# Kernel optimization log

Measured on AMD Instinct MI355X. Metric: run time of the kernel, lower is better.

Reference implementation:

```python
import jax, jax.numpy as jnp
import numpy as np

N, S, Q, P = 100000, 64, 50, 3  # pauli words, heads, qubits, pauli basis
EPS = 1e-12  # F.normalize clamp


def setup_inputs() -> dict:
    key = jax.random.key(0)
    k1, k2, k3, k4 = jax.random.split(key, 4)
    return {
        "batch_pauli_tensor": jax.random.uniform(k1, (N, Q, P), dtype=jnp.float32),
        "batch_coeff": jax.random.normal(k2, (N,), dtype=jnp.float32),
        "heads_param": jax.random.normal(k3, (S, Q, P), dtype=jnp.float32),
        "head_ratios_param": jax.random.normal(k4, (S,), dtype=jnp.float32),
    }


def reference(batch_pauli_tensor, batch_coeff, heads_param, head_ratios_param):
    s = heads_param.shape[0]
    heads = jax.nn.softplus(heads_param * 20.0)
    heads = heads / jnp.maximum(jnp.sum(heads, axis=-1, keepdims=True), EPS)
    hr = jax.nn.softplus(head_ratios_param * 20.0)
    hr = hr / jnp.maximum(jnp.sum(hr), EPS)
    hr = (hr + 0.001 / s) / 1.001
    # coverage: per-(word, head, qubit) match prob -> product over qubits -> ratio-weighted sum
    cov = jnp.einsum('nqp,sqp->nsq', batch_pauli_tensor, heads)  # [n, s, q]
    cov = jnp.prod(cov, axis=-1)                                 # [n, s]
    cov = jnp.einsum('s,ns->n', hr, cov)                         # [n]
    # variance loss
    return jnp.sum(batch_coeff ** 2 / cov)
```

## Files before the change

### kernel.cpp

```cpp
#include <hip/hip_runtime.h>
#include <math.h>

#define N_Q 50
#define N_P 3
#define N_S 64
#define ROW 150
#define BLK_ROWS 128
#define THREADS 256
#define SCHUNK 16

#define WS_CNT_OFF 6272
#define WS_HP_OFF 6336
#define WS_HRV_OFF 44736

__device__ __forceinline__ float softplus20(float x) {
    float z = x * 20.0f;
    return fmaxf(z, 0.0f) + log1pf(expf(-fabsf(z)));
}

__global__ void precompute_kernel(const float* __restrict__ heads_param,
                                  const float* __restrict__ hr_param,
                                  float* __restrict__ HP,
                                  float* __restrict__ hrv,
                                  int* __restrict__ cnt) {
    const int tid = threadIdx.x;
    if (blockIdx.x == 0) {
        if (tid == 0) *cnt = 0;
        if (tid < N_S) {
            float sp = softplus20(hr_param[tid]);
            float tot = sp;
            #pragma unroll
            for (int off = 32; off; off >>= 1) tot += __shfl_xor(tot, off);
            float hr = sp / fmaxf(tot, 1e-12f);
            hrv[tid] = (hr + 0.001f / (float)N_S) / 1.001f;
        }
    }
    int idx = blockIdx.x * blockDim.x + tid;
    if (idx < N_S * N_Q) {
        int q = idx / N_S;
        int s = idx - q * N_S;
        const float* hp = heads_param + ((size_t)s * N_Q + q) * N_P;
        float sp0 = softplus20(hp[0]);
        float sp1 = softplus20(hp[1]);
        float sp2 = softplus20(hp[2]);
        float denom = fmaxf(sp0 + sp1 + sp2, 1e-12f);
        float* o = HP + ((size_t)q * N_S + s) * 3;
        o[0] = sp0 / denom;
        o[1] = sp1 / denom;
        o[2] = sp2 / denom;
    }
}

__device__ __forceinline__ void computeQ2(const float4* __restrict__ Hq,
                                          float a0, float a1, float a2,
                                          float c0, float c1, float c2,
                                          float (&p)[SCHUNK], float (&p2)[SCHUNK]) {
    #pragma unroll
    for (int g = 0; g < 4; ++g) {
        float4 b0 = Hq[3 * g], b1 = Hq[3 * g + 1], b2 = Hq[3 * g + 2];
        p [4*g+0] *= fmaf(b0.x, a0, fmaf(b0.y, a1, b0.z * a2));
        p2[4*g+0] *= fmaf(b0.x, c0, fmaf(b0.y, c1, b0.z * c2));
        p [4*g+1] *= fmaf(b0.w, a0, fmaf(b1.x, a1, b1.y * a2));
        p2[4*g+1] *= fmaf(b0.w, c0, fmaf(b1.x, c1, b1.y * c2));
        p [4*g+2] *= fmaf(b1.z, a0, fmaf(b1.w, a1, b2.x * a2));
        p2[4*g+2] *= fmaf(b1.z, c0, fmaf(b1.w, c1, b2.x * c2));
        p [4*g+3] *= fmaf(b2.y, a0, fmaf(b2.z, a1, b2.w * a2));
        p2[4*g+3] *= fmaf(b2.y, c0, fmaf(b2.z, c1, b2.w * c2));
    }
}

__global__ __launch_bounds__(THREADS) void main_kernel(
    const float* __restrict__ A, const float* __restrict__ coeff,
    const float* __restrict__ HP, const float* __restrict__ hrv,
    double* __restrict__ partials, int* __restrict__ cnt,
    float* __restrict__ out, int N) {
    __shared__ float hHs[N_Q * N_S * 3];
    __shared__ float hrvl[N_S];
    __shared__ float covs[4][BLK_ROWS];
    __shared__ double redd[2];
    __shared__ int isLast;

    const int tid = threadIdx.x;
    const int lane = tid & 63;
    const int wave = tid >> 6;
    const int nbase = blockIdx.x * BLK_ROWS;

    for (int i = tid; i < (N_Q * N_S * 3) / 4; i += THREADS)
        ((float4*)hHs)[i] = ((const float4*)HP)[i];
    if (tid < N_S) hrvl[tid] = hrv[tid];
    __syncthreads();

    int n0 = nbase + lane;        if (n0 >= N) n0 = N - 1;
    int n1 = nbase + 64 + lane;   if (n1 >= N) n1 = N - 1;
    const float2* __restrict__ pA0 = (const float2*)A + (size_t)n0 * (ROW / 2);
    const float2* __restrict__ pA1 = (const float2*)A + (size_t)n1 * (ROW / 2);

    float prod0[SCHUNK], prod1[SCHUNK];
    #pragma unroll
    for (int i = 0; i < SCHUNK; ++i) { prod0[i] = 1.0f; prod1[i] = 1.0f; }

    const float4* __restrict__ Hbase = (const float4*)hHs + 12 * wave;

    #pragma unroll 5
    for (int w = 0; w < N_Q / 2; ++w) {
        float2 x0 = pA0[3 * w + 0], x1 = pA0[3 * w + 1], x2 = pA0[3 * w + 2];
        float2 y0 = pA1[3 * w + 0], y1 = pA1[3 * w + 1], y2 = pA1[3 * w + 2];
        const float4* Hq = Hbase + 96 * w;
        computeQ2(Hq,      x0.x, x0.y, x1.x,  y0.x, y0.y, y1.x, prod0, prod1);
        computeQ2(Hq + 48, x1.y, x2.x, x2.y,  y1.y, y2.x, y2.y, prod0, prod1);
    }

    float acc0 = 0.0f, acc1 = 0.0f;
    const int s0 = wave * SCHUNK;
    #pragma unroll
    for (int i = 0; i < SCHUNK; ++i) {
        float wgt = hrvl[s0 + i];
        acc0 = fmaf(wgt, prod0[i], acc0);
        acc1 = fmaf(wgt, prod1[i], acc1);
    }
    covs[wave][lane] = acc0;
    covs[wave][64 + lane] = acc1;
    __syncthreads();

    if (wave < 2) {
        const int row = wave * 64 + lane;
        const int n = nbase + row;
        float cov = covs[0][row] + covs[1][row] + covs[2][row] + covs[3][row];
        float term = 0.0f;
        if (n < N) { float c = coeff[n]; term = (c * c) / cov; }
        double td = (double)term;
        #pragma unroll
        for (int off = 32; off; off >>= 1) td += __shfl_down(td, off);
        if (lane == 0) redd[wave] = td;
    }
    __syncthreads();

    if (tid == 0) {
        partials[blockIdx.x] = redd[0] + redd[1];
        __threadfence();
        int v = atomicAdd(cnt, 1);
        isLast = (v == (int)gridDim.x - 1);
    }
    __syncthreads();

    if (isLast) {
        __threadfence();
        double s = 0.0;
        for (int i = tid; i < (int)gridDim.x; i += THREADS) s += partials[i];
        #pragma unroll
        for (int off = 32; off; off >>= 1) s += __shfl_down(s, off);
        __shared__ double redf[4];
        if (lane == 0) redf[wave] = s;
        __syncthreads();
        if (tid == 0) out[0] = (float)(redf[0] + redf[1] + redf[2] + redf[3]);
    }
}

extern "C" void kernel_launch(void* const* d_in, const int* in_sizes, int n_in,
                              void* d_out, int out_size, void* d_ws, size_t ws_size,
                              hipStream_t stream) {
    const float* A           = (const float*)d_in[0];
    const float* coeff       = (const float*)d_in[1];
    const float* heads_param = (const float*)d_in[2];
    const float* hr_param    = (const float*)d_in[3];
    const int N = in_sizes[1];
    const int nblocks = (N + BLK_ROWS - 1) / BLK_ROWS;

    char* ws = (char*)d_ws;
    double* partials = (double*)ws;
    int*   cnt = (int*)(ws + WS_CNT_OFF);
    float* HP  = (float*)(ws + WS_HP_OFF);
    float* hrv = (float*)(ws + WS_HRV_OFF);
    float* out = (float*)d_out;

    const int pre_blocks = (N_S * N_Q + THREADS - 1) / THREADS;
    precompute_kernel<<<pre_blocks, THREADS, 0, stream>>>(heads_param, hr_param,
                                                          HP, hrv, cnt);
    main_kernel<<<nblocks, THREADS, 0, stream>>>(A, coeff, HP, hrv, partials,
                                                 cnt, out, N);
}
```

Before: 154.1 us.

## Read head table via wave-uniform scalar loads instead of LDS staging

Drops the per-block copy of the 38KB normalized head table into shared memory. Each wave instead reads its slice straight from global memory through a readfirstlane-uniform pointer, which the compiler can turn into scalar loads. Rows per block are halved to 64 so each thread handles one row, and the next qubit group's inputs are software-prefetched. This removes the LDS fill and a barrier, at the cost of twice as many blocks, each reloading the heads from cache, and half the rows sharing each head-table read.

```diff
diff --git a/kernel.cpp b/kernel.cpp
--- a/kernel.cpp
+++ b/kernel.cpp
@@ -5,13 +5,14 @@
 #define N_P 3
 #define N_S 64
 #define ROW 150
-#define BLK_ROWS 128
+#define BLK_ROWS 64
 #define THREADS 256
+#define WAVES 4
 #define SCHUNK 16
 
-#define WS_CNT_OFF 6272
-#define WS_HP_OFF 6336
-#define WS_HRV_OFF 44736
+#define WS_CNT_OFF 12544
+#define WS_HP_OFF 12608
+#define WS_HRV_OFF 51008
 
 __device__ __forceinline__ float softplus20(float x) {
     float z = x * 20.0f;
@@ -51,21 +52,16 @@
     }
 }
 
-__device__ __forceinline__ void computeQ2(const float4* __restrict__ Hq,
+__device__ __forceinline__ void computeQ1(const float4* __restrict__ Hq,
                                           float a0, float a1, float a2,
-                                          float c0, float c1, float c2,
-                                          float (&p)[SCHUNK], float (&p2)[SCHUNK]) {
+                                          float (&p)[SCHUNK]) {
     #pragma unroll
     for (int g = 0; g < 4; ++g) {
         float4 b0 = Hq[3 * g], b1 = Hq[3 * g + 1], b2 = Hq[3 * g + 2];
-        p [4*g+0] *= fmaf(b0.x, a0, fmaf(b0.y, a1, b0.z * a2));
-        p2[4*g+0] *= fmaf(b0.x, c0, fmaf(b0.y, c1, b0.z * c2));
-        p [4*g+1] *= fmaf(b0.w, a0, fmaf(b1.x, a1, b1.y * a2));
-        p2[4*g+1] *= fmaf(b0.w, c0, fmaf(b1.x, c1, b1.y * c2));
-        p [4*g+2] *= fmaf(b1.z, a0, fmaf(b1.w, a1, b2.x * a2));
-        p2[4*g+2] *= fmaf(b1.z, c0, fmaf(b1.w, c1, b2.x * c2));
-        p [4*g+3] *= fmaf(b2.y, a0, fmaf(b2.z, a1, b2.w * a2));
-        p2[4*g+3] *= fmaf(b2.y, c0, fmaf(b2.z, c1, b2.w * c2));
+        p[4*g+0] *= fmaf(b0.x, a0, fmaf(b0.y, a1, b0.z * a2));
+        p[4*g+1] *= fmaf(b0.w, a0, fmaf(b1.x, a1, b1.y * a2));
+        p[4*g+2] *= fmaf(b1.z, a0, fmaf(b1.w, a1, b2.x * a2));
+        p[4*g+3] *= fmaf(b2.y, a0, fmaf(b2.z, a1, b2.w * a2));
     }
 }
 
@@ -74,69 +70,57 @@
     const float* __restrict__ HP, const float* __restrict__ hrv,
     double* __restrict__ partials, int* __restrict__ cnt,
     float* __restrict__ out, int N) {
-    __shared__ float hHs[N_Q * N_S * 3];
-    __shared__ float hrvl[N_S];
-    __shared__ float covs[4][BLK_ROWS];
-    __shared__ double redd[2];
+    __shared__ float covs[WAVES][BLK_ROWS];
+    __shared__ double redf[WAVES];
     __shared__ int isLast;
 
     const int tid = threadIdx.x;
     const int lane = tid & 63;
     const int wave = tid >> 6;
+    const int wq = __builtin_amdgcn_readfirstlane(wave);
     const int nbase = blockIdx.x * BLK_ROWS;
 
-    for (int i = tid; i < (N_Q * N_S * 3) / 4; i += THREADS)
-        ((float4*)hHs)[i] = ((const float4*)HP)[i];
-    if (tid < N_S) hrvl[tid] = hrv[tid];
-    __syncthreads();
+    int n0 = nbase + lane;  if (n0 >= N) n0 = N - 1;
+    const float2* __restrict__ pA0 = (const float2*)A + (size_t)n0 * (ROW / 2);
 
-    int n0 = nbase + lane;        if (n0 >= N) n0 = N - 1;
-    int n1 = nbase + 64 + lane;   if (n1 >= N) n1 = N - 1;
-    const float2* __restrict__ pA0 = (const float2*)A + (size_t)n0 * (ROW / 2);
-    const float2* __restrict__ pA1 = (const float2*)A + (size_t)n1 * (ROW / 2);
+    float prod[SCHUNK];
+    #pragma unroll
+    for (int i = 0; i < SCHUNK; ++i) prod[i] = 1.0f;
 
-    float prod0[SCHUNK], prod1[SCHUNK];
-    #pragma unroll
-    for (int i = 0; i < SCHUNK; ++i) { prod0[i] = 1.0f; prod1[i] = 1.0f; }
+    const float4* __restrict__ Hw = (const float4*)HP + 12 * wq;
 
-    const float4* __restrict__ Hbase = (const float4*)hHs + 12 * wave;
+    float2 x0 = pA0[0], x1 = pA0[1], x2 = pA0[2];
 
     #pragma unroll 5
     for (int w = 0; w < N_Q / 2; ++w) {
-        float2 x0 = pA0[3 * w + 0], x1 = pA0[3 * w + 1], x2 = pA0[3 * w + 2];
-        float2 y0 = pA1[3 * w + 0], y1 = pA1[3 * w + 1], y2 = pA1[3 * w + 2];
-        const float4* Hq = Hbase + 96 * w;
-        computeQ2(Hq,      x0.x, x0.y, x1.x,  y0.x, y0.y, y1.x, prod0, prod1);
-        computeQ2(Hq + 48, x1.y, x2.x, x2.y,  y1.y, y2.x, y2.y, prod0, prod1);
+        const int nb = (w < N_Q / 2 - 1) ? 3 * w + 3 : 0;
+        float2 nx0 = pA0[nb], nx1 = pA0[nb + 1], nx2 = pA0[nb + 2];
+        const float4* Hq = Hw + 96 * w;
+        computeQ1(Hq,      x0.x, x0.y, x1.x, prod);
+        computeQ1(Hq + 48, x1.y, x2.x, x2.y, prod);
+        x0 = nx0; x1 = nx1; x2 = nx2;
     }
 
-    float acc0 = 0.0f, acc1 = 0.0f;
-    const int s0 = wave * SCHUNK;
+    float acc = 0.0f;
+    const float* __restrict__ hw = hrv + SCHUNK * wq;
     #pragma unroll
-    for (int i = 0; i < SCHUNK; ++i) {
-        float wgt = hrvl[s0 + i];
-        acc0 = fmaf(wgt, prod0[i], acc0);
-        acc1 = fmaf(wgt, prod1[i], acc1);
-    }
-    covs[wave][lane] = acc0;
-    covs[wave][64 + lane] = acc1;
+    for (int i = 0; i < SCHUNK; ++i) acc = fmaf(hw[i], prod[i], acc);
+    covs[wave][lane] = acc;
     __syncthreads();
 
-    if (wave < 2) {
-        const int row = wave * 64 + lane;
-        const int n = nbase + row;
-        float cov = covs[0][row] + covs[1][row] + covs[2][row] + covs[3][row];
+    double td = 0.0;
+    if (wave == 0) {
+        float cov = covs[0][lane] + covs[1][lane] + covs[2][lane] + covs[3][lane];
         float term = 0.0f;
+        int n = nbase + lane;
         if (n < N) { float c = coeff[n]; term = (c * c) / cov; }
-        double td = (double)term;
+        td = (double)term;
         #pragma unroll
         for (int off = 32; off; off >>= 1) td += __shfl_down(td, off);
-        if (lane == 0) redd[wave] = td;
     }
-    __syncthreads();
 
     if (tid == 0) {
-        partials[blockIdx.x] = redd[0] + redd[1];
+        partials[blockIdx.x] = td;
         __threadfence();
         int v = atomicAdd(cnt, 1);
         isLast = (v == (int)gridDim.x - 1);
@@ -149,10 +133,14 @@
         for (int i = tid; i < (int)gridDim.x; i += THREADS) s += partials[i];
         #pragma unroll
         for (int off = 32; off; off >>= 1) s += __shfl_down(s, off);
-        __shared__ double redf[4];
         if (lane == 0) redf[wave] = s;
         __syncthreads();
-        if (tid == 0) out[0] = (float)(redf[0] + redf[1] + redf[2] + redf[3]);
+        if (tid == 0) {
+            double t = 0.0;
+            #pragma unroll
+            for (int wv = 0; wv < WAVES; ++wv) t += redf[wv];
+            out[0] = (float)t;
+        }
     }
 }
 
```

Measured after the change: 155.8 us. Within noise of the previous version (+1.1%).
